# Kernel optimization log

Hardware: AMD Instinct MI355X
Metric: run time of the kernel (lower is better)

Reference implementation:

```python
import jax, jax.numpy as jnp
import numpy as np

B, NVIS, NHID, NCLASS = 2048, 2048, 1024, 64


def setup_inputs() -> dict:
    key = jax.random.key(0)
    k1, k2, k3, k4, k5 = jax.random.split(key, 5)
    return {
        "v": jax.random.normal(k1, (B, NVIS), dtype=jnp.float32),
        "W": jax.random.normal(k2, (NVIS, NHID), dtype=jnp.float32),
        "c": jax.random.normal(k3, (1, NHID), dtype=jnp.float32),
        "d": jax.random.normal(k4, (1, NCLASS), dtype=jnp.float32),
        "U": jax.random.normal(k5, (NCLASS, NHID), dtype=jnp.float32),
    }


def reference(v, W, c, d, U):
    # precomputed_factor: [B, nhid]
    pre = jnp.matmul(v, W) + c
    # class free energies F[b, y] = d[0, y] + sum_j softplus(pre[b, j] + U[y, j])
    # broadcast to [B, nclass, nhid], reduce over hidden units
    F = d[0] + jnp.sum(jax.nn.softplus(pre[:, None, :] + U[None, :, :]), axis=-1)  # [B, nclass]
    # pairwise normalization 1 / sum_d exp(F_d - F_c) == softmax(F) along classes
    class_probs = jax.nn.softmax(F, axis=1)
    max_idx = jnp.argmax(class_probs, axis=1)
    one_hot = jax.nn.one_hot(max_idx, U.shape[0], dtype=jnp.int32)
    return class_probs, one_hot
```

## Files before the change

kernel.cpp:

```cpp
#include <hip/hip_runtime.h>

constexpr int kB    = 2048;
constexpr int kVIS  = 2048;
constexpr int kHID  = 1024;
constexpr int kCLS  = 64;
constexpr float kLog2e = 1.4426950408889634f;

typedef __attribute__((ext_vector_type(8))) short bf16x8;
typedef __attribute__((ext_vector_type(4))) float f32x4;
typedef __attribute__((ext_vector_type(2))) float f32x2;

typedef __attribute__((address_space(3))) unsigned       as3_u32;
typedef __attribute__((address_space(1))) const unsigned as1_u32;

__device__ __forceinline__ void g2lds16(const void* g, void* l) {
    __builtin_amdgcn_global_load_lds((as1_u32*)g, (as3_u32*)l, 16, 0, 0);
}

__device__ __forceinline__ unsigned short f2bf(float x) {
    unsigned u = __float_as_uint(x);
    u += 0x7fffu + ((u >> 16) & 1u);
    return (unsigned short)(u >> 16);
}
__device__ __forceinline__ float bf2f(unsigned short h) {
    return __uint_as_float(((unsigned)h) << 16);
}

__global__ __launch_bounds__(256) void prep_all(const float* __restrict__ v,
                                                const float* __restrict__ W,
                                                const float* __restrict__ U,
                                                unsigned short* __restrict__ vh,
                                                unsigned short* __restrict__ vl,
                                                unsigned short* __restrict__ wth,
                                                unsigned short* __restrict__ wtl,
                                                float* __restrict__ Utp) {
    __shared__ float T[32][33];
    const int bx = blockIdx.x;
    if (bx < 4096) {
        const int i = (bx * 256 + threadIdx.x) * 4;
        const float4 xv = *(const float4*)(v + i);
        ushort4 h, l;
        h.x = f2bf(xv.x); l.x = f2bf(xv.x - bf2f(h.x));
        h.y = f2bf(xv.y); l.y = f2bf(xv.y - bf2f(h.y));
        h.z = f2bf(xv.z); l.z = f2bf(xv.z - bf2f(h.z));
        h.w = f2bf(xv.w); l.w = f2bf(xv.w - bf2f(h.w));
        *(ushort4*)(vh + i) = h;
        *(ushort4*)(vl + i) = l;
    } else if (bx < 6144) {
        const int b = bx - 4096;
        const int n0 = (b & 31) * 32, k0 = (b >> 5) * 32;
        const int c = threadIdx.x & 31, r0 = threadIdx.x >> 5;
#pragma unroll
        for (int p = 0; p < 4; ++p) {
            const int r = r0 + p * 8;
            T[r][c] = W[(size_t)(k0 + r) * kHID + n0 + c];
        }
        __syncthreads();
#pragma unroll
        for (int p = 0; p < 4; ++p) {
            const int rr = r0 + p * 8;
            const float x = T[c][rr];
            const unsigned short h = f2bf(x);
            const unsigned short l = f2bf(x - bf2f(h));
            const size_t o = (size_t)(n0 + rr) * kVIS + k0 + c;
            wth[o] = h;
            wtl[o] = l;
        }
    } else {
        const int id = (bx - 6144) * 256 + threadIdx.x;
        const int j = id >> 6, y = id & 63;
        Utp[(((j >> 2) * kCLS + y) << 2) + (j & 3)] = U[(size_t)y * kHID + j] * kLog2e;
    }
}

__global__ __launch_bounds__(512, 4) void gemm_fused(const unsigned short* __restrict__ vh,
                                                     const unsigned short* __restrict__ vl,
                                                     const unsigned short* __restrict__ wth,
                                                     const unsigned short* __restrict__ wtl,
                                                     const float* __restrict__ cvec,
                                                     const float* __restrict__ Utp,
                                                     float* __restrict__ Fpart) {
    __shared__ __align__(16) union SMem {
        unsigned short stage[2][4][64 * 64];
        float psH[2][64][68];
    } smem;

    const int tid = threadIdx.x;
    const int lane = tid & 63, wave = tid >> 6;
    const int mh = wave >> 2;
    const int nh = (wave >> 1) & 1;
    const int kh = wave & 1;

    const int bid = blockIdx.x;
    const int idx = bid >> 3;
    const int mstripe = ((bid & 7) << 2) + (idx >> 4);
    const int ncol = idx & 15;
    const int m0 = mstripe * 64, n0 = ncol * 64;

    const int r = tid >> 3;
    const int oc = (((tid & 7) ^ ((tid >> 3) & 7)) << 3);
    const size_t ga = (size_t)(m0 + r) * kVIS + oc;
    const size_t gb = (size_t)(n0 + r) * kVIS + oc;
    const int ls = (r << 6) + ((tid & 7) << 3);

    const int fm = lane & 15, fq = lane >> 4;
    const int rx = fm & 7;
    const int ar0 = (mh * 32 + fm) << 6, ar1 = (mh * 32 + 16 + fm) << 6;
    const int br0 = (nh * 32 + fm) << 6, br1 = (nh * 32 + 16 + fm) << 6;
    const int p = (((kh << 2) + fq) ^ rx) << 3;

    f32x4 acc[2][2] = {};

    {
        g2lds16(vh + ga,  smem.stage[0][0] + ls);
        g2lds16(vl + ga,  smem.stage[0][1] + ls);
        g2lds16(wth + gb, smem.stage[0][2] + ls);
        g2lds16(wtl + gb, smem.stage[0][3] + ls);
    }
    __syncthreads();

    int cur = 0;
    for (int k0 = 0; k0 < kVIS; k0 += 64) {
        if (k0 + 64 < kVIS) {
            const int ko = k0 + 64;
            g2lds16(vh + ga + ko,  smem.stage[cur ^ 1][0] + ls);
            g2lds16(vl + ga + ko,  smem.stage[cur ^ 1][1] + ls);
            g2lds16(wth + gb + ko, smem.stage[cur ^ 1][2] + ls);
            g2lds16(wtl + gb + ko, smem.stage[cur ^ 1][3] + ls);
        }
        const unsigned short* Ah = smem.stage[cur][0];
        const unsigned short* Al = smem.stage[cur][1];
        const unsigned short* Bh = smem.stage[cur][2];
        const unsigned short* Bl = smem.stage[cur][3];
        const bf16x8 a_h0 = *(const bf16x8*)(Ah + ar0 + p);
        const bf16x8 a_h1 = *(const bf16x8*)(Ah + ar1 + p);
        const bf16x8 a_l0 = *(const bf16x8*)(Al + ar0 + p);
        const bf16x8 a_l1 = *(const bf16x8*)(Al + ar1 + p);
        const bf16x8 b_h0 = *(const bf16x8*)(Bh + br0 + p);
        const bf16x8 b_h1 = *(const bf16x8*)(Bh + br1 + p);
        const bf16x8 b_l0 = *(const bf16x8*)(Bl + br0 + p);
        const bf16x8 b_l1 = *(const bf16x8*)(Bl + br1 + p);
        acc[0][0] = __builtin_amdgcn_mfma_f32_16x16x32_bf16(a_h0, b_h0, acc[0][0], 0, 0, 0);
        acc[0][0] = __builtin_amdgcn_mfma_f32_16x16x32_bf16(a_h0, b_l0, acc[0][0], 0, 0, 0);
        acc[0][0] = __builtin_amdgcn_mfma_f32_16x16x32_bf16(a_l0, b_h0, acc[0][0], 0, 0, 0);
        acc[0][1] = __builtin_amdgcn_mfma_f32_16x16x32_bf16(a_h0, b_h1, acc[0][1], 0, 0, 0);
        acc[0][1] = __builtin_amdgcn_mfma_f32_16x16x32_bf16(a_h0, b_l1, acc[0][1], 0, 0, 0);
        acc[0][1] = __builtin_amdgcn_mfma_f32_16x16x32_bf16(a_l0, b_h1, acc[0][1], 0, 0, 0);
        acc[1][0] = __builtin_amdgcn_mfma_f32_16x16x32_bf16(a_h1, b_h0, acc[1][0], 0, 0, 0);
        acc[1][0] = __builtin_amdgcn_mfma_f32_16x16x32_bf16(a_h1, b_l0, acc[1][0], 0, 0, 0);
        acc[1][0] = __builtin_amdgcn_mfma_f32_16x16x32_bf16(a_l1, b_h0, acc[1][0], 0, 0, 0);
        acc[1][1] = __builtin_amdgcn_mfma_f32_16x16x32_bf16(a_h1, b_h1, acc[1][1], 0, 0, 0);
        acc[1][1] = __builtin_amdgcn_mfma_f32_16x16x32_bf16(a_h1, b_l1, acc[1][1], 0, 0, 0);
        acc[1][1] = __builtin_amdgcn_mfma_f32_16x16x32_bf16(a_l1, b_h1, acc[1][1], 0, 0, 0);
        __syncthreads();
        cur ^= 1;
    }

#pragma unroll
    for (int j = 0; j < 2; ++j) {
        const int col = nh * 32 + j * 16 + fm;
        const float cadd = kh ? 0.f : cvec[n0 + col];
#pragma unroll
        for (int i = 0; i < 2; ++i) {
            const int rbase = mh * 32 + i * 16 + fq * 4;
#pragma unroll
            for (int rr = 0; rr < 4; ++rr)
                smem.psH[kh][rbase + rr][col] = (acc[i][j][rr] + cadd) * kLog2e;
        }
    }
    __syncthreads();

#pragma unroll
    for (int s = 0; s < 2; ++s) {
        const int id = tid + (s << 9);
        const int row = id >> 4, q = id & 15;
        float4* d = (float4*)&smem.psH[0][row][q << 2];
        const float4* a = (const float4*)&smem.psH[1][row][q << 2];
        const float4 va = *a, vd = *d;
        *d = make_float4(vd.x + va.x, vd.y + va.y, vd.z + va.z, vd.w + va.w);
    }
    __syncthreads();

    const int q0 = (n0 >> 2);
    f32x2 relu2[8], prod2[8];
#pragma unroll
    for (int rr = 0; rr < 8; ++rr) { relu2[rr] = (f32x2)(0.f); prod2[rr] = (f32x2)(1.f); }

    const f32x2 zero2 = (f32x2)(0.f);
    for (int jc = 0; jc < 64; jc += 8) {
        const float4 ua = ((const float4*)Utp)[(q0 + (jc >> 2) + 0) * kCLS + lane];
        const float4 ub = ((const float4*)Utp)[(q0 + (jc >> 2) + 1) * kCLS + lane];
        const f32x2 u01 = {ua.x, ua.y}, u23 = {ua.z, ua.w};
        const f32x2 u45 = {ub.x, ub.y}, u67 = {ub.z, ub.w};
#pragma unroll
        for (int rr = 0; rr < 8; ++rr) {
            const int row = wave * 8 + rr;
            const float4 p0 = *(const float4*)&smem.psH[0][row][jc];
            const float4 p1 = *(const float4*)&smem.psH[0][row][jc + 4];
            f32x2 tp[4];
            tp[0] = (f32x2){p0.x, p0.y} + u01;
            tp[1] = (f32x2){p0.z, p0.w} + u23;
            tp[2] = (f32x2){p1.x, p1.y} + u45;
            tp[3] = (f32x2){p1.z, p1.w} + u67;
#pragma unroll
            for (int g = 0; g < 4; ++g) {
                const f32x2 t = tp[g];
                f32x2 e;
                e.x = __builtin_amdgcn_exp2f(-__builtin_fabsf(t.x));
                e.y = __builtin_amdgcn_exp2f(-__builtin_fabsf(t.y));
                prod2[rr] = __builtin_elementwise_fma(prod2[rr], e, prod2[rr]);
                relu2[rr] += __builtin_elementwise_max(t, zero2);
            }
        }
    }
#pragma unroll
    for (int rr = 0; rr < 8; ++rr) {
        const float contrib = relu2[rr].x + relu2[rr].y +
                              __builtin_amdgcn_logf(prod2[rr].x * prod2[rr].y);
        Fpart[((size_t)ncol * kB + m0 + wave * 8 + rr) * kCLS + lane] = contrib;
    }
}

__global__ __launch_bounds__(256) void softmax_final(const float* __restrict__ Fpart,
                                                     const float* __restrict__ dvec,
                                                     float* __restrict__ out) {
    const int tid = threadIdx.x;
    const int lane = tid & 63, wave = tid >> 6;
    const int row = blockIdx.x * 4 + wave;
    double s = 0.0;
#pragma unroll
    for (int k = 0; k < kHID / 64; ++k)
        s += (double)Fpart[((size_t)k * kB + row) * kCLS + lane];
    const float G = (float)s + dvec[lane] * kLog2e;

    float m = G;
    int mi = lane;
#pragma unroll
    for (int off = 32; off; off >>= 1) {
        const float om = __shfl_xor(m, off);
        const int   oi = __shfl_xor(mi, off);
        if (om > m || (om == m && oi < mi)) { m = om; mi = oi; }
    }
    const float e2 = __builtin_amdgcn_exp2f(G - m);
    float ssum = e2;
#pragma unroll
    for (int off = 32; off; off >>= 1) ssum += __shfl_xor(ssum, off);
    out[(size_t)row * kCLS + lane] = e2 / ssum;
    out[(size_t)kB * kCLS + (size_t)row * kCLS + lane] = (lane == mi) ? 1.0f : 0.0f;
}

constexpr int BM = 64, BN = 64, BK = 16;

__global__ __launch_bounds__(256) void gemm_vw(const float* __restrict__ V,
                                               const float* __restrict__ Wm,
                                               const float* __restrict__ cvec,
                                               float* __restrict__ pre) {
    __shared__ float As[BK][BM + 4];
    __shared__ float Bs[BK][BN + 4];
    const int tid = threadIdx.x;
    const int tx = tid & 15, ty = tid >> 4;
    const int m0 = blockIdx.y * BM, n0 = blockIdx.x * BN;
    const int arow = tid >> 2, acol = (tid & 3) << 2;
    const int brow = tid >> 4, bcol = (tid & 15) << 2;
    const float* vptr = V + (size_t)(m0 + arow) * kVIS + acol;
    const float* wptr = Wm + (size_t)brow * kHID + n0 + bcol;
    float acc[4][4] = {};
    for (int k0 = 0; k0 < kVIS; k0 += BK) {
        const float4 a4 = *(const float4*)(vptr + k0);
        const float4 b4 = *(const float4*)(wptr + (size_t)k0 * kHID);
        __syncthreads();
        As[acol + 0][arow] = a4.x; As[acol + 1][arow] = a4.y;
        As[acol + 2][arow] = a4.z; As[acol + 3][arow] = a4.w;
        *(float4*)&Bs[brow][bcol] = b4;
        __syncthreads();
#pragma unroll
        for (int k = 0; k < BK; ++k) {
            const float4 av = *(const float4*)&As[k][ty << 2];
            const float4 bv = *(const float4*)&Bs[k][tx << 2];
            const float a[4] = {av.x, av.y, av.z, av.w};
            const float b[4] = {bv.x, bv.y, bv.z, bv.w};
#pragma unroll
            for (int i = 0; i < 4; ++i)
#pragma unroll
                for (int j = 0; j < 4; ++j) acc[i][j] += a[i] * b[j];
        }
    }
#pragma unroll
    for (int i = 0; i < 4; ++i) {
        const int row = m0 + (ty << 2) + i;
        const int col = n0 + (tx << 2);
        const float4 cv = *(const float4*)(cvec + col);
        float4 o;
        o.x = acc[i][0] + cv.x; o.y = acc[i][1] + cv.y;
        o.z = acc[i][2] + cv.z; o.w = acc[i][3] + cv.w;
        *(float4*)(pre + (size_t)row * kHID + col) = o;
    }
}

__device__ __forceinline__ float softplus_f(float x) {
    return fmaxf(x, 0.f) + __logf(1.f + __expf(-fabsf(x)));
}

__global__ __launch_bounds__(256) void classify(const float* __restrict__ pre,
                                                const float* __restrict__ U,
                                                const float* __restrict__ dvec,
                                                float* __restrict__ out) {
    __shared__ float preS[4][kHID];
    __shared__ float Fs[4][kCLS];
    const int tid = threadIdx.x;
    const int lane = tid & 63, wave = tid >> 6;
    const int b0 = blockIdx.x * 4;
    const float4* src = (const float4*)(pre + (size_t)b0 * kHID);
    float4* dst = (float4*)preS;
    for (int i = tid; i < kHID; i += 256) dst[i] = src[i];
    __syncthreads();
    for (int yi = 0; yi < 16; ++yi) {
        const int y = (wave << 4) + yi;
        const float* Uy = U + (size_t)y * kHID;
        float a0 = 0.f, a1 = 0.f, a2 = 0.f, a3 = 0.f;
#pragma unroll
        for (int it = 0; it < kHID / 64; ++it) {
            const int j = lane + (it << 6);
            const float u = Uy[j];
            a0 += softplus_f(preS[0][j] + u);
            a1 += softplus_f(preS[1][j] + u);
            a2 += softplus_f(preS[2][j] + u);
            a3 += softplus_f(preS[3][j] + u);
        }
        double d0 = a0, d1 = a1, d2 = a2, d3 = a3;
#pragma unroll
        for (int off = 32; off; off >>= 1) {
            d0 += __shfl_xor(d0, off); d1 += __shfl_xor(d1, off);
            d2 += __shfl_xor(d2, off); d3 += __shfl_xor(d3, off);
        }
        if (lane == 0) {
            const float dy = dvec[y];
            Fs[0][y] = (float)d0 + dy; Fs[1][y] = (float)d1 + dy;
            Fs[2][y] = (float)d2 + dy; Fs[3][y] = (float)d3 + dy;
        }
    }
    __syncthreads();
    const float F = Fs[wave][lane];
    float m = F; int mi = lane;
#pragma unroll
    for (int off = 32; off; off >>= 1) {
        const float om = __shfl_xor(m, off);
        const int oi = __shfl_xor(mi, off);
        if (om > m || (om == m && oi < mi)) { m = om; mi = oi; }
    }
    const float e = __expf(F - m);
    float s = e;
#pragma unroll
    for (int off = 32; off; off >>= 1) s += __shfl_xor(s, off);
    const int row = b0 + wave;
    out[(size_t)row * kCLS + lane] = e / s;
    out[(size_t)kB * kCLS + (size_t)row * kCLS + lane] = (lane == mi) ? 1.0f : 0.0f;
}

extern "C" void kernel_launch(void* const* d_in, const int* in_sizes, int n_in,
                              void* d_out, int out_size, void* d_ws, size_t ws_size,
                              hipStream_t stream) {
    const float* v = (const float*)d_in[0];
    const float* W = (const float*)d_in[1];
    const float* c = (const float*)d_in[2];
    const float* d = (const float*)d_in[3];
    const float* U = (const float*)d_in[4];
    float* out = (float*)d_out;
    char* ws = (char*)d_ws;

    const size_t need = 33816576;
    if (ws_size >= need) {
        unsigned short* vh  = (unsigned short*)(ws);
        unsigned short* vl  = (unsigned short*)(ws + 8388608);
        unsigned short* wth = (unsigned short*)(ws + 16777216);
        unsigned short* wtl = (unsigned short*)(ws + 20971520);
        float* Utp   = (float*)(ws + 25165824);
        float* Fpart = (float*)(ws + 25427968);
        prep_all<<<6400, 256, 0, stream>>>(v, W, U, vh, vl, wth, wtl, Utp);
        gemm_fused<<<512, 512, 0, stream>>>(vh, vl, wth, wtl, c, Utp, Fpart);
        softmax_final<<<kB / 4, 256, 0, stream>>>(Fpart, d, out);
    } else {
        float* pre = (float*)ws;
        gemm_vw<<<dim3(kHID / BN, kB / BM), 256, 0, stream>>>(v, W, c, pre);
        classify<<<kB / 4, 256, 0, stream>>>(pre, U, d, out);
    }
}
```

Measured before the change: 127.3 us.

## Halve GEMM block to four waves each covering all 64 rows; enlarge W transpose tiles

The fused GEMM now runs with 256 threads instead of 512. Each wave computes all 64 M rows for its N half and K half, so every B fragment is reused across four A fragments and each thread issues two async global-to-LDS loads per buffer. The softplus epilogue has each wave handle 16 rows. Separately, the W transpose/split prep uses 64x64 tiles with fewer blocks. This trades fewer waves per CU and more registers per thread for better fragment reuse and fewer barriers per unit of work.

```diff
diff --git a/kernel.cpp b/kernel.cpp
--- a/kernel.cpp
+++ b/kernel.cpp
@@ -34,7 +34,7 @@
                                                 unsigned short* __restrict__ wth,
                                                 unsigned short* __restrict__ wtl,
                                                 float* __restrict__ Utp) {
-    __shared__ float T[32][33];
+    __shared__ float T[64][65];
     const int bx = blockIdx.x;
     if (bx < 4096) {
         const int i = (bx * 256 + threadIdx.x) * 4;
@@ -46,34 +46,35 @@
         h.w = f2bf(xv.w); l.w = f2bf(xv.w - bf2f(h.w));
         *(ushort4*)(vh + i) = h;
         *(ushort4*)(vl + i) = l;
-    } else if (bx < 6144) {
+    } else if (bx < 4608) {
         const int b = bx - 4096;
-        const int n0 = (b & 31) * 32, k0 = (b >> 5) * 32;
-        const int c = threadIdx.x & 31, r0 = threadIdx.x >> 5;
-#pragma unroll
-        for (int p = 0; p < 4; ++p) {
-            const int r = r0 + p * 8;
+        const int n0 = (b & 15) * 64;
+        const int k0 = (b >> 4) * 64;
+        const int c = threadIdx.x & 63, r0 = threadIdx.x >> 6;
+#pragma unroll
+        for (int ps = 0; ps < 16; ++ps) {
+            const int r = r0 + ps * 4;
             T[r][c] = W[(size_t)(k0 + r) * kHID + n0 + c];
         }
         __syncthreads();
 #pragma unroll
-        for (int p = 0; p < 4; ++p) {
-            const int rr = r0 + p * 8;
-            const float x = T[c][rr];
+        for (int ps = 0; ps < 16; ++ps) {
+            const int nn = r0 + ps * 4;
+            const float x = T[c][nn];
             const unsigned short h = f2bf(x);
             const unsigned short l = f2bf(x - bf2f(h));
-            const size_t o = (size_t)(n0 + rr) * kVIS + k0 + c;
+            const size_t o = (size_t)(n0 + nn) * kVIS + k0 + c;
             wth[o] = h;
             wtl[o] = l;
         }
     } else {
-        const int id = (bx - 6144) * 256 + threadIdx.x;
+        const int id = (bx - 4608) * 256 + threadIdx.x;
         const int j = id >> 6, y = id & 63;
         Utp[(((j >> 2) * kCLS + y) << 2) + (j & 3)] = U[(size_t)y * kHID + j] * kLog2e;
     }
 }
 
-__global__ __launch_bounds__(512, 4) void gemm_fused(const unsigned short* __restrict__ vh,
+__global__ __launch_bounds__(256, 2) void gemm_fused(const unsigned short* __restrict__ vh,
                                                      const unsigned short* __restrict__ vl,
                                                      const unsigned short* __restrict__ wth,
                                                      const unsigned short* __restrict__ wtl,
@@ -87,9 +88,8 @@
 
     const int tid = threadIdx.x;
     const int lane = tid & 63, wave = tid >> 6;
-    const int mh = wave >> 2;
-    const int nh = (wave >> 1) & 1;
-    const int kh = wave & 1;
+    const int nh = wave & 1;
+    const int kh = wave >> 1;
 
     const int bid = blockIdx.x;
     const int idx = bid >> 3;
@@ -98,24 +98,31 @@
     const int m0 = mstripe * 64, n0 = ncol * 64;
 
     const int r = tid >> 3;
-    const int oc = (((tid & 7) ^ ((tid >> 3) & 7)) << 3);
-    const size_t ga = (size_t)(m0 + r) * kVIS + oc;
-    const size_t gb = (size_t)(n0 + r) * kVIS + oc;
-    const int ls = (r << 6) + ((tid & 7) << 3);
+    const int oc = (((tid & 7) ^ (r & 7)) << 3);
+    const size_t ga0 = (size_t)(m0 + r) * kVIS + oc;
+    const size_t ga1 = ga0 + (size_t)32 * kVIS;
+    const size_t gb0 = (size_t)(n0 + r) * kVIS + oc;
+    const size_t gb1 = gb0 + (size_t)32 * kVIS;
+    const int ls0 = (r << 6) + ((tid & 7) << 3);
+    const int ls1 = ls0 + (32 << 6);
 
     const int fm = lane & 15, fq = lane >> 4;
     const int rx = fm & 7;
-    const int ar0 = (mh * 32 + fm) << 6, ar1 = (mh * 32 + 16 + fm) << 6;
+    const int ar0 = (fm) << 6, ar1 = (16 + fm) << 6, ar2 = (32 + fm) << 6, ar3 = (48 + fm) << 6;
     const int br0 = (nh * 32 + fm) << 6, br1 = (nh * 32 + 16 + fm) << 6;
     const int p = (((kh << 2) + fq) ^ rx) << 3;
 
-    f32x4 acc[2][2] = {};
+    f32x4 acc[4][2] = {};
 
     {
-        g2lds16(vh + ga,  smem.stage[0][0] + ls);
-        g2lds16(vl + ga,  smem.stage[0][1] + ls);
-        g2lds16(wth + gb, smem.stage[0][2] + ls);
-        g2lds16(wtl + gb, smem.stage[0][3] + ls);
+        g2lds16(vh + ga0,  smem.stage[0][0] + ls0);
+        g2lds16(vh + ga1,  smem.stage[0][0] + ls1);
+        g2lds16(vl + ga0,  smem.stage[0][1] + ls0);
+        g2lds16(vl + ga1,  smem.stage[0][1] + ls1);
+        g2lds16(wth + gb0, smem.stage[0][2] + ls0);
+        g2lds16(wth + gb1, smem.stage[0][2] + ls1);
+        g2lds16(wtl + gb0, smem.stage[0][3] + ls0);
+        g2lds16(wtl + gb1, smem.stage[0][3] + ls1);
     }
     __syncthreads();
 
@@ -123,10 +130,14 @@
     for (int k0 = 0; k0 < kVIS; k0 += 64) {
         if (k0 + 64 < kVIS) {
             const int ko = k0 + 64;
-            g2lds16(vh + ga + ko,  smem.stage[cur ^ 1][0] + ls);
-            g2lds16(vl + ga + ko,  smem.stage[cur ^ 1][1] + ls);
-            g2lds16(wth + gb + ko, smem.stage[cur ^ 1][2] + ls);
-            g2lds16(wtl + gb + ko, smem.stage[cur ^ 1][3] + ls);
+            g2lds16(vh + ga0 + ko,  smem.stage[cur ^ 1][0] + ls0);
+            g2lds16(vh + ga1 + ko,  smem.stage[cur ^ 1][0] + ls1);
+            g2lds16(vl + ga0 + ko,  smem.stage[cur ^ 1][1] + ls0);
+            g2lds16(vl + ga1 + ko,  smem.stage[cur ^ 1][1] + ls1);
+            g2lds16(wth + gb0 + ko, smem.stage[cur ^ 1][2] + ls0);
+            g2lds16(wth + gb1 + ko, smem.stage[cur ^ 1][2] + ls1);
+            g2lds16(wtl + gb0 + ko, smem.stage[cur ^ 1][3] + ls0);
+            g2lds16(wtl + gb1 + ko, smem.stage[cur ^ 1][3] + ls1);
         }
         const unsigned short* Ah = smem.stage[cur][0];
         const unsigned short* Al = smem.stage[cur][1];
@@ -134,24 +145,40 @@
         const unsigned short* Bl = smem.stage[cur][3];
         const bf16x8 a_h0 = *(const bf16x8*)(Ah + ar0 + p);
         const bf16x8 a_h1 = *(const bf16x8*)(Ah + ar1 + p);
+        const bf16x8 a_h2 = *(const bf16x8*)(Ah + ar2 + p);
+        const bf16x8 a_h3 = *(const bf16x8*)(Ah + ar3 + p);
         const bf16x8 a_l0 = *(const bf16x8*)(Al + ar0 + p);
         const bf16x8 a_l1 = *(const bf16x8*)(Al + ar1 + p);
+        const bf16x8 a_l2 = *(const bf16x8*)(Al + ar2 + p);
+        const bf16x8 a_l3 = *(const bf16x8*)(Al + ar3 + p);
         const bf16x8 b_h0 = *(const bf16x8*)(Bh + br0 + p);
         const bf16x8 b_h1 = *(const bf16x8*)(Bh + br1 + p);
         const bf16x8 b_l0 = *(const bf16x8*)(Bl + br0 + p);
         const bf16x8 b_l1 = *(const bf16x8*)(Bl + br1 + p);
         acc[0][0] = __builtin_amdgcn_mfma_f32_16x16x32_bf16(a_h0, b_h0, acc[0][0], 0, 0, 0);
+        acc[0][1] = __builtin_amdgcn_mfma_f32_16x16x32_bf16(a_h0, b_h1, acc[0][1], 0, 0, 0);
+        acc[1][0] = __builtin_amdgcn_mfma_f32_16x16x32_bf16(a_h1, b_h0, acc[1][0], 0, 0, 0);
+        acc[1][1] = __builtin_amdgcn_mfma_f32_16x16x32_bf16(a_h1, b_h1, acc[1][1], 0, 0, 0);
+        acc[2][0] = __builtin_amdgcn_mfma_f32_16x16x32_bf16(a_h2, b_h0, acc[2][0], 0, 0, 0);
+        acc[2][1] = __builtin_amdgcn_mfma_f32_16x16x32_bf16(a_h2, b_h1, acc[2][1], 0, 0, 0);
+        acc[3][0] = __builtin_amdgcn_mfma_f32_16x16x32_bf16(a_h3, b_h0, acc[3][0], 0, 0, 0);
+        acc[3][1] = __builtin_amdgcn_mfma_f32_16x16x32_bf16(a_h3, b_h1, acc[3][1], 0, 0, 0);
         acc[0][0] = __builtin_amdgcn_mfma_f32_16x16x32_bf16(a_h0, b_l0, acc[0][0], 0, 0, 0);
+        acc[0][1] = __builtin_amdgcn_mfma_f32_16x16x32_bf16(a_h0, b_l1, acc[0][1], 0, 0, 0);
+        acc[1][0] = __builtin_amdgcn_mfma_f32_16x16x32_bf16(a_h1, b_l0, acc[1][0], 0, 0, 0);
+        acc[1][1] = __builtin_amdgcn_mfma_f32_16x16x32_bf16(a_h1, b_l1, acc[1][1], 0, 0, 0);
+        acc[2][0] = __builtin_amdgcn_mfma_f32_16x16x32_bf16(a_h2, b_l0, acc[2][0], 0, 0, 0);
+        acc[2][1] = __builtin_amdgcn_mfma_f32_16x16x32_bf16(a_h2, b_l1, acc[2][1], 0, 0, 0);
+        acc[3][0] = __builtin_amdgcn_mfma_f32_16x16x32_bf16(a_h3, b_l0, acc[3][0], 0, 0, 0);
+        acc[3][1] = __builtin_amdgcn_mfma_f32_16x16x32_bf16(a_h3, b_l1, acc[3][1], 0, 0, 0);
         acc[0][0] = __builtin_amdgcn_mfma_f32_16x16x32_bf16(a_l0, b_h0, acc[0][0], 0, 0, 0);
-        acc[0][1] = __builtin_amdgcn_mfma_f32_16x16x32_bf16(a_h0, b_h1, acc[0][1], 0, 0, 0);
-        acc[0][1] = __builtin_amdgcn_mfma_f32_16x16x32_bf16(a_h0, b_l1, acc[0][1], 0, 0, 0);
         acc[0][1] = __builtin_amdgcn_mfma_f32_16x16x32_bf16(a_l0, b_h1, acc[0][1], 0, 0, 0);
-        acc[1][0] = __builtin_amdgcn_mfma_f32_16x16x32_bf16(a_h1, b_h0, acc[1][0], 0, 0, 0);
-        acc[1][0] = __builtin_amdgcn_mfma_f32_16x16x32_bf16(a_h1, b_l0, acc[1][0], 0, 0, 0);
         acc[1][0] = __builtin_amdgcn_mfma_f32_16x16x32_bf16(a_l1, b_h0, acc[1][0], 0, 0, 0);
-        acc[1][1] = __builtin_amdgcn_mfma_f32_16x16x32_bf16(a_h1, b_h1, acc[1][1], 0, 0, 0);
-        acc[1][1] = __builtin_amdgcn_mfma_f32_16x16x32_bf16(a_h1, b_l1, acc[1][1], 0, 0, 0);
         acc[1][1] = __builtin_amdgcn_mfma_f32_16x16x32_bf16(a_l1, b_h1, acc[1][1], 0, 0, 0);
+        acc[2][0] = __builtin_amdgcn_mfma_f32_16x16x32_bf16(a_l2, b_h0, acc[2][0], 0, 0, 0);
+        acc[2][1] = __builtin_amdgcn_mfma_f32_16x16x32_bf16(a_l2, b_h1, acc[2][1], 0, 0, 0);
+        acc[3][0] = __builtin_amdgcn_mfma_f32_16x16x32_bf16(a_l3, b_h0, acc[3][0], 0, 0, 0);
+        acc[3][1] = __builtin_amdgcn_mfma_f32_16x16x32_bf16(a_l3, b_h1, acc[3][1], 0, 0, 0);
         __syncthreads();
         cur ^= 1;
     }
@@ -161,8 +188,8 @@
         const int col = nh * 32 + j * 16 + fm;
         const float cadd = kh ? 0.f : cvec[n0 + col];
 #pragma unroll
-        for (int i = 0; i < 2; ++i) {
-            const int rbase = mh * 32 + i * 16 + fq * 4;
+        for (int i = 0; i < 4; ++i) {
+            const int rbase = i * 16 + fq * 4;
 #pragma unroll
             for (int rr = 0; rr < 4; ++rr)
                 smem.psH[kh][rbase + rr][col] = (acc[i][j][rr] + cadd) * kLog2e;
@@ -171,8 +198,8 @@
     __syncthreads();
 
 #pragma unroll
-    for (int s = 0; s < 2; ++s) {
-        const int id = tid + (s << 9);
+    for (int s = 0; s < 4; ++s) {
+        const int id = tid + (s << 8);
         const int row = id >> 4, q = id & 15;
         float4* d = (float4*)&smem.psH[0][row][q << 2];
         const float4* a = (const float4*)&smem.psH[1][row][q << 2];
@@ -182,9 +209,9 @@
     __syncthreads();
 
     const int q0 = (n0 >> 2);
-    f32x2 relu2[8], prod2[8];
-#pragma unroll
-    for (int rr = 0; rr < 8; ++rr) { relu2[rr] = (f32x2)(0.f); prod2[rr] = (f32x2)(1.f); }
+    f32x2 relu2[16], prod2[16];
+#pragma unroll
+    for (int rr = 0; rr < 16; ++rr) { relu2[rr] = (f32x2)(0.f); prod2[rr] = (f32x2)(1.f); }
 
     const f32x2 zero2 = (f32x2)(0.f);
     for (int jc = 0; jc < 64; jc += 8) {
@@ -193,8 +220,8 @@
         const f32x2 u01 = {ua.x, ua.y}, u23 = {ua.z, ua.w};
         const f32x2 u45 = {ub.x, ub.y}, u67 = {ub.z, ub.w};
 #pragma unroll
-        for (int rr = 0; rr < 8; ++rr) {
-            const int row = wave * 8 + rr;
+        for (int rr = 0; rr < 16; ++rr) {
+            const int row = wave * 16 + rr;
             const float4 p0 = *(const float4*)&smem.psH[0][row][jc];
             const float4 p1 = *(const float4*)&smem.psH[0][row][jc + 4];
             f32x2 tp[4];
@@ -214,10 +241,10 @@
         }
     }
 #pragma unroll
-    for (int rr = 0; rr < 8; ++rr) {
+    for (int rr = 0; rr < 16; ++rr) {
         const float contrib = relu2[rr].x + relu2[rr].y +
                               __builtin_amdgcn_logf(prod2[rr].x * prod2[rr].y);
-        Fpart[((size_t)ncol * kB + m0 + wave * 8 + rr) * kCLS + lane] = contrib;
+        Fpart[((size_t)ncol * kB + m0 + wave * 16 + rr) * kCLS + lane] = contrib;
     }
 }
 
@@ -376,8 +403,8 @@
         unsigned short* wtl = (unsigned short*)(ws + 20971520);
         float* Utp   = (float*)(ws + 25165824);
         float* Fpart = (float*)(ws + 25427968);
-        prep_all<<<6400, 256, 0, stream>>>(v, W, U, vh, vl, wth, wtl, Utp);
-        gemm_fused<<<512, 512, 0, stream>>>(vh, vl, wth, wtl, c, Utp, Fpart);
+        prep_all<<<4864, 256, 0, stream>>>(v, W, U, vh, vl, wth, wtl, Utp);
+        gemm_fused<<<512, 256, 0, stream>>>(vh, vl, wth, wtl, c, Utp, Fpart);
         softmax_final<<<kB / 4, 256, 0, stream>>>(Fpart, d, out);
     } else {
         float* pre = (float*)ws;
```

Result: slower. 131.7 us (+3.5%).

## Remap softplus epilogue to row-per-lane, class-per-wave and enlarge W transpose tiles

Applied to the files above, without the earlier changes.

The fused GEMM epilogue now assigns one row per lane and eight classes per wave, reading U rows directly in a plain scaled row-major layout with float4 vectors. Results are transposed through LDS before being stored to Fpart. The prep kernel transposes W in 64x64 tiles instead of 32x32, and converts U with vectorised float4 copies instead of a scattered permuted layout. The aim is fewer LDS reads per exp, wider vector math, and fewer prep blocks. The cost is an extra LDS round-trip with a barrier, plus a U read pattern that is uniform across lanes (broadcast) but touches several rows.

```diff
diff --git a/kernel.cpp b/kernel.cpp
--- a/kernel.cpp
+++ b/kernel.cpp
@@ -8,7 +8,6 @@
 
 typedef __attribute__((ext_vector_type(8))) short bf16x8;
 typedef __attribute__((ext_vector_type(4))) float f32x4;
-typedef __attribute__((ext_vector_type(2))) float f32x2;
 
 typedef __attribute__((address_space(3))) unsigned       as3_u32;
 typedef __attribute__((address_space(1))) const unsigned as1_u32;
@@ -34,7 +33,7 @@
                                                 unsigned short* __restrict__ wth,
                                                 unsigned short* __restrict__ wtl,
                                                 float* __restrict__ Utp) {
-    __shared__ float T[32][33];
+    __shared__ float T[64][65];
     const int bx = blockIdx.x;
     if (bx < 4096) {
         const int i = (bx * 256 + threadIdx.x) * 4;
@@ -46,30 +45,34 @@
         h.w = f2bf(xv.w); l.w = f2bf(xv.w - bf2f(h.w));
         *(ushort4*)(vh + i) = h;
         *(ushort4*)(vl + i) = l;
-    } else if (bx < 6144) {
+    } else if (bx < 4608) {
         const int b = bx - 4096;
-        const int n0 = (b & 31) * 32, k0 = (b >> 5) * 32;
-        const int c = threadIdx.x & 31, r0 = threadIdx.x >> 5;
-#pragma unroll
-        for (int p = 0; p < 4; ++p) {
-            const int r = r0 + p * 8;
+        const int n0 = (b & 15) * 64;
+        const int k0 = (b >> 4) * 64;
+        const int c = threadIdx.x & 63, r0 = threadIdx.x >> 6;
+#pragma unroll
+        for (int ps = 0; ps < 16; ++ps) {
+            const int r = r0 + ps * 4;
             T[r][c] = W[(size_t)(k0 + r) * kHID + n0 + c];
         }
         __syncthreads();
 #pragma unroll
-        for (int p = 0; p < 4; ++p) {
-            const int rr = r0 + p * 8;
-            const float x = T[c][rr];
+        for (int ps = 0; ps < 16; ++ps) {
+            const int nn = r0 + ps * 4;
+            const float x = T[c][nn];
             const unsigned short h = f2bf(x);
             const unsigned short l = f2bf(x - bf2f(h));
-            const size_t o = (size_t)(n0 + rr) * kVIS + k0 + c;
+            const size_t o = (size_t)(n0 + nn) * kVIS + k0 + c;
             wth[o] = h;
             wtl[o] = l;
         }
     } else {
-        const int id = (bx - 6144) * 256 + threadIdx.x;
-        const int j = id >> 6, y = id & 63;
-        Utp[(((j >> 2) * kCLS + y) << 2) + (j & 3)] = U[(size_t)y * kHID + j] * kLog2e;
+        const int id = (bx - 4608) * 256 + threadIdx.x;
+        const float4 u = ((const float4*)U)[id];
+        float4 o;
+        o.x = u.x * kLog2e; o.y = u.y * kLog2e;
+        o.z = u.z * kLog2e; o.w = u.w * kLog2e;
+        ((float4*)Utp)[id] = o;
     }
 }
 
@@ -181,42 +184,40 @@
     }
     __syncthreads();
 
-    const int q0 = (n0 >> 2);
-    f32x2 relu2[8], prod2[8];
-#pragma unroll
-    for (int rr = 0; rr < 8; ++rr) { relu2[rr] = (f32x2)(0.f); prod2[rr] = (f32x2)(1.f); }
-
-    const f32x2 zero2 = (f32x2)(0.f);
-    for (int jc = 0; jc < 64; jc += 8) {
-        const float4 ua = ((const float4*)Utp)[(q0 + (jc >> 2) + 0) * kCLS + lane];
-        const float4 ub = ((const float4*)Utp)[(q0 + (jc >> 2) + 1) * kCLS + lane];
-        const f32x2 u01 = {ua.x, ua.y}, u23 = {ua.z, ua.w};
-        const f32x2 u45 = {ub.x, ub.y}, u67 = {ub.z, ub.w};
-#pragma unroll
-        for (int rr = 0; rr < 8; ++rr) {
-            const int row = wave * 8 + rr;
-            const float4 p0 = *(const float4*)&smem.psH[0][row][jc];
-            const float4 p1 = *(const float4*)&smem.psH[0][row][jc + 4];
-            f32x2 tp[4];
-            tp[0] = (f32x2){p0.x, p0.y} + u01;
-            tp[1] = (f32x2){p0.z, p0.w} + u23;
-            tp[2] = (f32x2){p1.x, p1.y} + u45;
-            tp[3] = (f32x2){p1.z, p1.w} + u67;
-#pragma unroll
-            for (int g = 0; g < 4; ++g) {
-                const f32x2 t = tp[g];
-                f32x2 e;
-                e.x = __builtin_amdgcn_exp2f(-__builtin_fabsf(t.x));
-                e.y = __builtin_amdgcn_exp2f(-__builtin_fabsf(t.y));
-                prod2[rr] = __builtin_elementwise_fma(prod2[rr], e, prod2[rr]);
-                relu2[rr] += __builtin_elementwise_max(t, zero2);
-            }
-        }
-    }
+    const int y0 = wave * 8;
+    f32x4 relu[8], prod[8];
+#pragma unroll
+    for (int yy = 0; yy < 8; ++yy) { relu[yy] = (f32x4)(0.f); prod[yy] = (f32x4)(1.f); }
+
+    const f32x4 zero4 = (f32x4)(0.f);
+    for (int jq = 0; jq < 16; ++jq) {
+        const f32x4 p4 = *(const f32x4*)&smem.psH[0][lane][jq << 2];
+#pragma unroll
+        for (int yy = 0; yy < 8; ++yy) {
+            const f32x4 u4 = *(const f32x4*)(Utp + (size_t)(y0 + yy) * kHID + n0 + (jq << 2));
+            const f32x4 t = p4 + u4;
+            f32x4 e;
+            e.x = __builtin_amdgcn_exp2f(-__builtin_fabsf(t.x));
+            e.y = __builtin_amdgcn_exp2f(-__builtin_fabsf(t.y));
+            e.z = __builtin_amdgcn_exp2f(-__builtin_fabsf(t.z));
+            e.w = __builtin_amdgcn_exp2f(-__builtin_fabsf(t.w));
+            prod[yy] = __builtin_elementwise_fma(prod[yy], e, prod[yy]);
+            relu[yy] += __builtin_elementwise_max(t, zero4);
+        }
+    }
+
+    float* Fs = (float*)&smem.psH[1][0][0];
+#pragma unroll
+    for (int yy = 0; yy < 8; ++yy) {
+        const float rsum = relu[yy].x + relu[yy].y + relu[yy].z + relu[yy].w;
+        const float pp = prod[yy].x * prod[yy].y * prod[yy].z * prod[yy].w;
+        Fs[lane * 65 + y0 + yy] = rsum + __builtin_amdgcn_logf(pp);
+    }
+    __syncthreads();
+
 #pragma unroll
     for (int rr = 0; rr < 8; ++rr) {
-        const float contrib = relu2[rr].x + relu2[rr].y +
-                              __builtin_amdgcn_logf(prod2[rr].x * prod2[rr].y);
+        const float contrib = Fs[(wave * 8 + rr) * 65 + lane];
         Fpart[((size_t)ncol * kB + m0 + wave * 8 + rr) * kCLS + lane] = contrib;
     }
 }
@@ -376,7 +377,7 @@
         unsigned short* wtl = (unsigned short*)(ws + 20971520);
         float* Utp   = (float*)(ws + 25165824);
         float* Fpart = (float*)(ws + 25427968);
-        prep_all<<<6400, 256, 0, stream>>>(v, W, U, vh, vl, wth, wtl, Utp);
+        prep_all<<<4672, 256, 0, stream>>>(v, W, U, vh, vl, wth, wtl, Utp);
         gemm_fused<<<512, 512, 0, stream>>>(vh, vl, wth, wtl, c, Utp, Fpart);
         softmax_final<<<kB / 4, 256, 0, stream>>>(Fpart, d, out);
     } else {
```

Result: slower. 135.9 us (+6.8%).
